# Kernel tuning notes

Hardware: AMD Instinct MI355X
Metric: run time of the kernel (lower is better)

The kernel has to match this reference:

```python
import jax, jax.numpy as jnp
import numpy as np

S, D, H, HD, FF = 4096, 1024, 16, 64, 4096  # seq, d_embed, heads, head_dim, hidden
EPS = 1e-6  # flax LayerNorm default epsilon


def layer_norm(x, scale, bias):
    mu = jnp.mean(x, axis=-1, keepdims=True)
    var = jnp.var(x, axis=-1, keepdims=True)
    return (x - mu) * jax.lax.rsqrt(var + EPS) * scale + bias


def rope(x):
    # x: [S, H, HD]; standard half-split rotary embedding, base 10000
    half = x.shape[-1] // 2
    freq = 1.0 / (10000.0 ** (jnp.arange(half, dtype=x.dtype) / half))  # [half]
    ang = jnp.arange(x.shape[0], dtype=x.dtype)[:, None] * freq          # [S, half]
    cos = jnp.cos(ang)[:, None, :]
    sin = jnp.sin(ang)[:, None, :]
    x1, x2 = x[..., :half], x[..., half:]
    return jnp.concatenate([x1 * cos - x2 * sin, x2 * cos + x1 * sin], axis=-1)


def setup_inputs() -> dict:
    key = jax.random.key(0)
    ks = jax.random.split(key, 8)
    s = 0.02
    return {
        "x": jax.random.normal(ks[0], (S, D), jnp.float32),
        "ln1_scale": jnp.ones((D,), jnp.float32), "ln1_bias": jnp.zeros((D,), jnp.float32),
        "ln2_scale": jnp.ones((D,), jnp.float32), "ln2_bias": jnp.zeros((D,), jnp.float32),
        "Wq": jax.random.normal(ks[1], (D, H, HD), jnp.float32) * s, "bq": jnp.zeros((H, HD), jnp.float32),
        "Wk": jax.random.normal(ks[2], (D, H, HD), jnp.float32) * s, "bk": jnp.zeros((H, HD), jnp.float32),
        "Wv": jax.random.normal(ks[3], (D, H, HD), jnp.float32) * s, "bv": jnp.zeros((H, HD), jnp.float32),
        "Wo": jax.random.normal(ks[4], (H, HD, D), jnp.float32) * s, "bo": jnp.zeros((D,), jnp.float32),
        "W1": jax.random.normal(ks[5], (D, FF), jnp.float32) * s, "b1": jnp.zeros((FF,), jnp.float32),
        "W2": jax.random.normal(ks[6], (FF, D), jnp.float32) * s, "b2": jnp.zeros((D,), jnp.float32),
    }


def reference(x, ln1_scale, ln1_bias, ln2_scale, ln2_bias, Wq, bq, Wk, bk, Wv, bv, Wo, bo, W1, b1, W2, b2):
    # Pre-LN attention block with RoPE fused into QK scores
    y = layer_norm(x, ln1_scale, ln1_bias)
    q = jnp.einsum('sd,dhc->shc', y, Wq) + bq  # [S,H,HD]
    k = jnp.einsum('sd,dhc->shc', y, Wk) + bk
    v = jnp.einsum('sd,dhc->shc', y, Wv) + bv
    q = rope(q)
    k = rope(k)
    scores = jnp.einsum('qhc,khc->hqk', q, k) / jnp.sqrt(jnp.asarray(HD, x.dtype))  # [H,S,S]
    p = jax.nn.softmax(scores, axis=-1)
    o = jnp.einsum('hqk,khc->qhc', p, v)                # [S,H,HD]
    attn_out = jnp.einsum('qhc,hcd->qd', o, Wo) + bo    # [S,D]
    x = x + attn_out
    # Pre-LN GELU MLP block
    y = layer_norm(x, ln2_scale, ln2_bias)
    y = jax.nn.gelu(y @ W1 + b1, approximate=False)
    x = x + (y @ W2 + b2)
    return x
```

## Files before the change

kernel.cpp:

```cpp
#include <hip/hip_runtime.h>
#include <hip/hip_bf16.h>
#include <math.h>

using bf16 = __hip_bfloat16;
typedef __attribute__((ext_vector_type(8))) short short8;
typedef __attribute__((ext_vector_type(4))) short s16x4;
typedef __attribute__((ext_vector_type(4))) float f32x4;

constexpr int S = 4096, D = 1024, H = 16, HD = 64, FF = 4096;

static __device__ __forceinline__ float tof(bf16 v) { return __bfloat162float(v); }
static __device__ __forceinline__ bf16 tob(float v) { return __float2bfloat16(v); }
static __device__ __forceinline__ short tobs(float v) {
    bf16 h = __float2bfloat16(v);
    return *reinterpret_cast<short*>(&h);
}
static __device__ __forceinline__ unsigned pkbf16(float a, float b) {
    __hip_bfloat162 h = __float22bfloat162_rn(make_float2(a, b));
    return *reinterpret_cast<unsigned*>(&h);
}

static __device__ __forceinline__ f32x4 mfma16(short8 a, short8 b, f32x4 c) {
    return __builtin_amdgcn_mfma_f32_16x16x32_bf16(a, b, c, 0, 0, 0);
}
static __device__ __forceinline__ void stage16(const bf16* g, bf16* l) {
    __builtin_amdgcn_global_load_lds((__attribute__((address_space(1))) void*)g,
                                     (__attribute__((address_space(3))) void*)l, 16, 0, 0);
}

__global__ __launch_bounds__(256) void ln_kernel(const float* __restrict__ x,
                                                 const float* __restrict__ scale,
                                                 const float* __restrict__ bias,
                                                 bf16* __restrict__ y) {
    int row = blockIdx.x, t = threadIdx.x;
    const float* xr = x + (size_t)row * D;
    float v[4], s = 0.f, ss = 0.f;
#pragma unroll
    for (int i = 0; i < 4; ++i) {
        v[i] = xr[t + 256 * i];
        s += v[i]; ss += v[i] * v[i];
    }
    __shared__ float r0[256], r1[256];
    r0[t] = s; r1[t] = ss;
    __syncthreads();
    for (int off = 128; off; off >>= 1) {
        if (t < off) { r0[t] += r0[t + off]; r1[t] += r1[t + off]; }
        __syncthreads();
    }
    float mu  = r0[0] * (1.f / D);
    float var = r1[0] * (1.f / D) - mu * mu;
    float inv = rsqrtf(var + 1e-6f);
    bf16* yr = y + (size_t)row * D;
#pragma unroll
    for (int i = 0; i < 4; ++i) {
        int c = t + 256 * i;
        yr[c] = tob((v[i] - mu) * inv * scale[c] + bias[c]);
    }
}

__global__ __launch_bounds__(256) void wtrans(const float* __restrict__ W,
                                              bf16* __restrict__ BT, int K, int N) {
    __shared__ float t[32][33];
    int kt = blockIdx.y * 32, nt = blockIdx.x * 32;
    int tid = threadIdx.x, r = tid >> 5, c = tid & 31;
#pragma unroll
    for (int p = 0; p < 4; ++p)
        t[r + p * 8][c] = W[(size_t)(kt + r + p * 8) * N + nt + c];
    __syncthreads();
#pragma unroll
    for (int p = 0; p < 4; ++p)
        BT[(size_t)(nt + r + p * 8) * K + kt + c] = tob(t[c][r + p * 8]);
}

__global__ __launch_bounds__(256) void wtrans_qkv(const float* __restrict__ Wq,
                                                  const float* __restrict__ Wk,
                                                  const float* __restrict__ Wv,
                                                  bf16* __restrict__ BT) {
    __shared__ float t[32][33];
    const float* W = blockIdx.z == 0 ? Wq : (blockIdx.z == 1 ? Wk : Wv);
    bf16* dst = BT + (size_t)blockIdx.z * 1024 * 1024;
    int kt = blockIdx.y * 32, nt = blockIdx.x * 32;
    int tid = threadIdx.x, r = tid >> 5, c = tid & 31;
#pragma unroll
    for (int p = 0; p < 4; ++p)
        t[r + p * 8][c] = W[(size_t)(kt + r + p * 8) * 1024 + nt + c];
    __syncthreads();
#pragma unroll
    for (int p = 0; p < 4; ++p)
        dst[(size_t)(nt + r + p * 8) * 1024 + kt + c] = tob(t[c][r + p * 8]);
}

__global__ void bconcat(const float* __restrict__ bq, const float* __restrict__ bk,
                        const float* __restrict__ bv, float* __restrict__ out) {
    int i = blockIdx.x * 256 + threadIdx.x;
    out[i] = i < 1024 ? bq[i] : (i < 2048 ? bk[i - 1024] : bv[i - 2048]);
}

#define EPI_NONE 0
#define EPI_RES  1
#define EPI_GELU 2

template <int EPI, int MT>
__global__ __launch_bounds__(256, MT == 128 ? 2 : 3) void gemm_bt(
    const bf16* __restrict__ A, const bf16* __restrict__ BT,
    const float* __restrict__ bias, const float* resid, void* out,
    int M, int N, int K) {
    constexpr int NJ = (MT == 128) ? 4 : 2;
    __shared__ bf16 As[MT * 32];
    __shared__ bf16 Bs[128 * 32];
    const int tid = threadIdx.x;
    const int w = tid >> 6, lane = tid & 63;
    const int quad = lane >> 4, l16 = lane & 15;
    const int rowBase = blockIdx.y * MT, colBase = blockIdx.x * 128;
    const int wr = (MT == 128) ? (w >> 1) * 64 : 0;
    const int wc = (MT == 128) ? (w & 1) * 64 : w * 32;
    const int sr = lane >> 2, skb = (lane & 3) * 8;
    f32x4 acc[4][NJ] = {};
    for (int k0 = 0; k0 < K; k0 += 32) {
        __syncthreads();
        if (MT == 128) {
#pragma unroll
            for (int t = 0; t < 2; ++t) {
                int inst = w * 2 + t;
                int r = inst * 16 + sr;
                stage16(A  + (size_t)(rowBase + r) * K + k0 + skb, As + inst * 512);
                stage16(BT + (size_t)(colBase + r) * K + k0 + skb, Bs + inst * 512);
            }
        } else {
            stage16(A + (size_t)(rowBase + w * 16 + sr) * K + k0 + skb, As + w * 512);
#pragma unroll
            for (int t = 0; t < 2; ++t) {
                int inst = w + t * 4;
                stage16(BT + (size_t)(colBase + inst * 16 + sr) * K + k0 + skb, Bs + inst * 512);
            }
        }
        __syncthreads();
        const bf16* pa = As + (wr + l16) * 32 + quad * 8;
        const bf16* pb = Bs + (wc + l16) * 32 + quad * 8;
        short8 a[4], b[NJ];
#pragma unroll
        for (int i = 0; i < 4; ++i) a[i] = *(const short8*)(pa + i * 512);
#pragma unroll
        for (int j = 0; j < NJ; ++j) b[j] = *(const short8*)(pb + j * 512);
#pragma unroll
        for (int i = 0; i < 4; ++i)
#pragma unroll
            for (int j = 0; j < NJ; ++j) acc[i][j] = mfma16(a[i], b[j], acc[i][j]);
    }
#pragma unroll
    for (int j = 0; j < NJ; ++j) {
        int c = colBase + wc + j * 16 + l16;
        float bj = bias[c];
#pragma unroll
        for (int i = 0; i < 4; ++i) {
            int r0 = rowBase + wr + i * 16 + quad * 4;
#pragma unroll
            for (int reg = 0; reg < 4; ++reg) {
                size_t idx = (size_t)(r0 + reg) * N + c;
                float val = acc[i][j][reg] + bj;
                if (EPI == EPI_NONE) {
                    ((bf16*)out)[idx] = tob(val);
                } else if (EPI == EPI_RES) {
                    ((float*)out)[idx] = val + resid[idx];
                } else {
                    float g = 0.5f * val * (1.f + erff(val * 0.70710678118f));
                    ((bf16*)out)[idx] = tob(g);
                }
            }
        }
    }
}

__global__ __launch_bounds__(256) void rope_kernel(bf16* __restrict__ QKV) {
    int idx = blockIdx.x * 256 + threadIdx.x;
    int s = idx >> 9, rem = idx & 511, h = rem >> 5, c = rem & 31;
    float freq = __expf(-(float)c * (9.210340371976184f / 32.f));
    float ang = (float)s * freq, sn, cs;
    sincosf(ang, &sn, &cs);
    const float qs = 0.125f * 1.44269504088896f;
    size_t base = (size_t)s * 3072 + h * 64 + c;
    float q1 = tof(QKV[base]), q2 = tof(QKV[base + 32]);
    QKV[base]      = tob((q1 * cs - q2 * sn) * qs);
    QKV[base + 32] = tob((q2 * cs + q1 * sn) * qs);
    float k1 = tof(QKV[base + 1024]), k2 = tof(QKV[base + 1056]);
    QKV[base + 1024] = tob(k1 * cs - k2 * sn);
    QKV[base + 1056] = tob(k2 * cs + k1 * sn);
}

__global__ __launch_bounds__(256) void vtrans(const short* __restrict__ QKV,
                                              short* __restrict__ VT) {
    int h = blockIdx.y, st = blockIdx.x * 64;
    __shared__ short t[64][72];
    int tid = threadIdx.x, r0 = tid >> 3, c0 = (tid & 7) * 8;
#pragma unroll
    for (int p = 0; p < 2; ++p) {
        int r = r0 + p * 32;
        short8 d = *(const short8*)(QKV + (size_t)(st + r) * 3072 + 2048 + h * 64 + c0);
#pragma unroll
        for (int j = 0; j < 8; ++j) t[r][c0 + j] = d[j];
    }
    __syncthreads();
#pragma unroll
    for (int p = 0; p < 2; ++p) {
        int c = r0 + p * 32;
        short8 v;
#pragma unroll
        for (int j = 0; j < 8; ++j) v[j] = t[c0 + j][c];
        *(short8*)(VT + ((size_t)h * 64 + c) * 4096 + st + c0) = v;
    }
}

__global__ __launch_bounds__(256, 4) void attn_kernel(const bf16* __restrict__ QKV,
                                                      const bf16* __restrict__ VT,
                                                      bf16* __restrict__ O) {
    const int h = blockIdx.x >> 6, qb = blockIdx.x & 63;
    const int w = threadIdx.x >> 6, lane = threadIdx.x & 63;
    const int quad = lane >> 4, l16 = lane & 15;
    const int q0w = qb * 64 + w * 16;
    const bf16* Qh = QKV + h * 64;
    const bf16* Kh = QKV + 1024 + h * 64;
    const bf16* Vh = VT + (size_t)h * 64 * 4096;

    __shared__ char smem[24576];
    bf16* Ks = (bf16*)(smem);
    bf16* Vs = (bf16*)(smem + 8192);
    char* Pb = smem + 16384 + w * 2048;

    const int sw = l16 & 7;
    const int rloc = lane >> 3, slot = lane & 7;
    const int schunk = (slot ^ rloc) * 8;

    short8 qf[2];
#pragma unroll
    for (int c = 0; c < 2; ++c)
        qf[c] = *(const short8*)(Qh + (size_t)(q0w + l16) * 3072 + c * 32 + quad * 8);

    const short ob = (l16 == 0) ? (short)0x3F80 : (short)0;
    const short8 ones8 = {ob, ob, ob, ob, ob, ob, ob, ob};

    f32x4 acc[4] = {};
    f32x4 accl = {};
    const f32x4 zero = {0.f, 0.f, 0.f, 0.f};

    for (int kt = 0; kt < 4096; kt += 64) {
        __syncthreads();
        {
            int r = (2 * w ) * 8 + rloc;
            stage16(Kh + (size_t)(kt + r) * 3072 + schunk, Ks + 2 * w * 512);
            stage16(Vh + (size_t)r * 4096 + kt + schunk, Vs + 2 * w * 512);
            int r1 = (2 * w + 1) * 8 + rloc;
            stage16(Kh + (size_t)(kt + r1) * 3072 + schunk, Ks + (2 * w + 1) * 512);
            stage16(Vh + (size_t)r1 * 4096 + kt + schunk, Vs + (2 * w + 1) * 512);
        }
        __syncthreads();

        f32x4 st[4];
#pragma unroll
        for (int nt = 0; nt < 4; ++nt) {
            const bf16* kr = Ks + (nt * 16 + l16) * 64;
            short8 k0 = *(const short8*)(kr + ((quad ^ sw) * 8));
            short8 k1 = *(const short8*)(kr + (((quad + 4) ^ sw) * 8));
            st[nt] = mfma16(k1, qf[1], mfma16(k0, qf[0], zero));
        }
#pragma unroll
        for (int nt = 0; nt < 4; ++nt) {
            float e0 = exp2f(st[nt][0]), e1 = exp2f(st[nt][1]);
            float e2 = exp2f(st[nt][2]), e3 = exp2f(st[nt][3]);
            uint2 pk = {pkbf16(e0, e1), pkbf16(e2, e3)};
            *(uint2*)(Pb + l16 * 128 + (((nt * 2 + (quad >> 1)) ^ sw) * 16) + (quad & 1) * 8) = pk;
        }
        asm volatile("s_waitcnt lgkmcnt(0)" ::: "memory");
#pragma unroll
        for (int c = 0; c < 2; ++c) {
            short8 pB = *(const short8*)(Pb + l16 * 128 + (((c * 4 + quad) ^ sw) * 16));
            accl = mfma16(ones8, pB, accl);
#pragma unroll
            for (int vt = 0; vt < 4; ++vt) {
                short8 vf = *(const short8*)(Vs + (vt * 16 + l16) * 64 + (((c * 4 + quad) ^ sw) * 8));
                acc[vt] = mfma16(vf, pB, acc[vt]);
            }
        }
    }
    float linv = 1.f / __shfl(accl[0], l16, 64);
#pragma unroll
    for (int vt = 0; vt < 4; ++vt) {
        s16x4 ov = {tobs(acc[vt][0] * linv), tobs(acc[vt][1] * linv),
                    tobs(acc[vt][2] * linv), tobs(acc[vt][3] * linv)};
        *(s16x4*)(O + (size_t)(q0w + l16) * 1024 + h * 64 + vt * 16 + quad * 4) = ov;
    }
}

extern "C" void kernel_launch(void* const* d_in, const int* in_sizes, int n_in,
                              void* d_out, int out_size, void* d_ws, size_t ws_size,
                              hipStream_t stream) {
    const float* x   = (const float*)d_in[0];
    const float* s1  = (const float*)d_in[1];
    const float* b1n = (const float*)d_in[2];
    const float* s2  = (const float*)d_in[3];
    const float* b2n = (const float*)d_in[4];
    const float* Wq  = (const float*)d_in[5];
    const float* bq  = (const float*)d_in[6];
    const float* Wk  = (const float*)d_in[7];
    const float* bk  = (const float*)d_in[8];
    const float* Wv  = (const float*)d_in[9];
    const float* bv  = (const float*)d_in[10];
    const float* Wo  = (const float*)d_in[11];
    const float* bo  = (const float*)d_in[12];
    const float* W1  = (const float*)d_in[13];
    const float* b1  = (const float*)d_in[14];
    const float* W2  = (const float*)d_in[15];
    const float* b2  = (const float*)d_in[16];

    char* ws = (char*)d_ws;
    bf16*  y     = (bf16*)(ws);
    bf16*  QKV   = (bf16*)(ws + (8ull  << 20));
    bf16*  o     = (bf16*)(ws + (32ull << 20));
    bf16*  hb    = (bf16*)(ws + (40ull << 20));
    bf16*  BTqkv = (bf16*)(ws + (40ull << 20));
    bf16*  BTo   = (bf16*)(ws + (46ull << 20));
    bf16*  VT    = (bf16*)(ws + (72ull << 20));
    bf16*  BT1   = (bf16*)(ws + (82ull << 20));
    float* bqkv  = (float*)(ws + (90ull << 20));
    bf16*  BT2   = y;
    float* x1    = (float*)d_out;

    wtrans_qkv<<<dim3(32, 32, 3), 256, 0, stream>>>(Wq, Wk, Wv, BTqkv);
    wtrans<<<dim3(32, 32),  256, 0, stream>>>(Wo, BTo, D, D);
    wtrans<<<dim3(128, 32), 256, 0, stream>>>(W1, BT1, D, FF);
    bconcat<<<12, 256, 0, stream>>>(bq, bk, bv, bqkv);

    ln_kernel<<<S, 256, 0, stream>>>(x, s1, b1n, y);

    gemm_bt<EPI_NONE, 128><<<dim3(24, 32), 256, 0, stream>>>(y, BTqkv, bqkv, nullptr, QKV, S, 3072, D);

    rope_kernel<<<(S * H * 32) / 256, 256, 0, stream>>>(QKV);
    vtrans<<<dim3(64, 16), 256, 0, stream>>>((const short*)QKV, (short*)VT);

    attn_kernel<<<H * 64, 256, 0, stream>>>(QKV, VT, o);

    gemm_bt<EPI_RES, 64><<<dim3(8, 64), 256, 0, stream>>>(o, BTo, bo, x, x1, S, D, D);

    ln_kernel<<<S, 256, 0, stream>>>(x1, s2, b2n, y);

    gemm_bt<EPI_GELU, 128><<<dim3(32, 32), 256, 0, stream>>>(y, BT1, b1, nullptr, hb, S, FF, D);

    wtrans<<<dim3(32, 128), 256, 0, stream>>>(W2, BT2, FF, D);
    gemm_bt<EPI_RES, 64><<<dim3(8, 64), 256, 0, stream>>>(hb, BT2, b2, x1, d_out, S, D, FF);
}
```

Baseline: 477.8 us.

## Fuse RoPE and V transpose into QKV GEMM, double-buffer attention, merge weight transposes

Applies rotary embedding and the V transpose directly in the QKV GEMM epilogue, removing two separate kernels and their extra passes over the QKV buffer. All weight transposes and the bias concat become a single launch. The attention loop double-buffers K/V tiles in shared memory so loads overlap compute, at the cost of more LDS, and uses the hardware exp2 intrinsic. The epilogue now does per-element sincos and strided stores, which may add epilogue cost.

```diff
diff --git a/kernel.cpp b/kernel.cpp
--- a/kernel.cpp
+++ b/kernel.cpp
@@ -19,6 +19,12 @@
     __hip_bfloat162 h = __float22bfloat162_rn(make_float2(a, b));
     return *reinterpret_cast<unsigned*>(&h);
 }
+
+#if __has_builtin(__builtin_amdgcn_exp2f)
+#define EXP2(x) __builtin_amdgcn_exp2f(x)
+#else
+#define EXP2(x) exp2f(x)
+#endif
 
 static __device__ __forceinline__ f32x4 mfma16(short8 a, short8 b, f32x4 c) {
     return __builtin_amdgcn_mfma_f32_16x16x32_bf16(a, b, c, 0, 0, 0);
@@ -58,10 +64,29 @@
     }
 }
 
-__global__ __launch_bounds__(256) void wtrans(const float* __restrict__ W,
-                                              bf16* __restrict__ BT, int K, int N) {
+__global__ __launch_bounds__(256) void wtrans_all(
+    const float* __restrict__ Wq, const float* __restrict__ Wk,
+    const float* __restrict__ Wv, const float* __restrict__ Wo,
+    const float* __restrict__ W1, const float* __restrict__ W2,
+    const float* __restrict__ bq, const float* __restrict__ bk,
+    const float* __restrict__ bv,
+    bf16* __restrict__ BTqkv, bf16* __restrict__ BTo,
+    bf16* __restrict__ BT1, bf16* __restrict__ BT2, float* __restrict__ bqkv) {
+    int id = blockIdx.x;
+    if (id >= 12288) {
+        int i = (id - 12288) * 256 + threadIdx.x;
+        bqkv[i] = i < 1024 ? bq[i] : (i < 2048 ? bk[i - 1024] : bv[i - 2048]);
+        return;
+    }
+    const float* W; bf16* dst; int K, N, local;
+    if (id < 3072)      { int s = id >> 10; W = s == 0 ? Wq : (s == 1 ? Wk : Wv);
+                          dst = BTqkv + (size_t)s * 1048576; K = 1024; N = 1024; local = id & 1023; }
+    else if (id < 4096) { W = Wo; dst = BTo; K = 1024; N = 1024; local = id - 3072; }
+    else if (id < 8192) { W = W1; dst = BT1; K = 1024; N = 4096; local = id - 4096; }
+    else                { W = W2; dst = BT2; K = 4096; N = 1024; local = id - 8192; }
+    int ls = (N == 4096) ? 7 : 5;
+    int nt = (local & ((1 << ls) - 1)) << 5, kt = (local >> ls) << 5;
     __shared__ float t[32][33];
-    int kt = blockIdx.y * 32, nt = blockIdx.x * 32;
     int tid = threadIdx.x, r = tid >> 5, c = tid & 31;
 #pragma unroll
     for (int p = 0; p < 4; ++p)
@@ -69,41 +94,17 @@
     __syncthreads();
 #pragma unroll
     for (int p = 0; p < 4; ++p)
-        BT[(size_t)(nt + r + p * 8) * K + kt + c] = tob(t[c][r + p * 8]);
-}
-
-__global__ __launch_bounds__(256) void wtrans_qkv(const float* __restrict__ Wq,
-                                                  const float* __restrict__ Wk,
-                                                  const float* __restrict__ Wv,
-                                                  bf16* __restrict__ BT) {
-    __shared__ float t[32][33];
-    const float* W = blockIdx.z == 0 ? Wq : (blockIdx.z == 1 ? Wk : Wv);
-    bf16* dst = BT + (size_t)blockIdx.z * 1024 * 1024;
-    int kt = blockIdx.y * 32, nt = blockIdx.x * 32;
-    int tid = threadIdx.x, r = tid >> 5, c = tid & 31;
-#pragma unroll
-    for (int p = 0; p < 4; ++p)
-        t[r + p * 8][c] = W[(size_t)(kt + r + p * 8) * 1024 + nt + c];
-    __syncthreads();
-#pragma unroll
-    for (int p = 0; p < 4; ++p)
-        dst[(size_t)(nt + r + p * 8) * 1024 + kt + c] = tob(t[c][r + p * 8]);
-}
-
-__global__ void bconcat(const float* __restrict__ bq, const float* __restrict__ bk,
-                        const float* __restrict__ bv, float* __restrict__ out) {
-    int i = blockIdx.x * 256 + threadIdx.x;
-    out[i] = i < 1024 ? bq[i] : (i < 2048 ? bk[i - 1024] : bv[i - 2048]);
-}
-
-#define EPI_NONE 0
+        dst[(size_t)(nt + r + p * 8) * K + kt + c] = tob(t[c][r + p * 8]);
+}
+
 #define EPI_RES  1
 #define EPI_GELU 2
+#define EPI_QKV  3
 
 template <int EPI, int MT>
 __global__ __launch_bounds__(256, MT == 128 ? 2 : 3) void gemm_bt(
     const bf16* __restrict__ A, const bf16* __restrict__ BT,
-    const float* __restrict__ bias, const float* resid, void* out,
+    const float* __restrict__ bias, const float* resid, void* out, void* out2,
     int M, int N, int K) {
     constexpr int NJ = (MT == 128) ? 4 : 2;
     __shared__ bf16 As[MT * 32];
@@ -147,66 +148,68 @@
 #pragma unroll
             for (int j = 0; j < NJ; ++j) acc[i][j] = mfma16(a[i], b[j], acc[i][j]);
     }
-#pragma unroll
-    for (int j = 0; j < NJ; ++j) {
-        int c = colBase + wc + j * 16 + l16;
-        float bj = bias[c];
-#pragma unroll
-        for (int i = 0; i < 4; ++i) {
-            int r0 = rowBase + wr + i * 16 + quad * 4;
-#pragma unroll
-            for (int reg = 0; reg < 4; ++reg) {
-                size_t idx = (size_t)(r0 + reg) * N + c;
-                float val = acc[i][j][reg] + bj;
-                if (EPI == EPI_NONE) {
-                    ((bf16*)out)[idx] = tob(val);
-                } else if (EPI == EPI_RES) {
-                    ((float*)out)[idx] = val + resid[idx];
-                } else {
-                    float g = 0.5f * val * (1.f + erff(val * 0.70710678118f));
-                    ((bf16*)out)[idx] = tob(g);
+    if (EPI == EPI_QKV) {
+        bf16* QKVo = (bf16*)out;
+        bf16* VTo  = (bf16*)out2;
+        if (colBase >= 2048) {
+#pragma unroll
+            for (int j = 0; j < NJ; ++j) {
+                int c = colBase + wc + j * 16 + l16;
+                float bj = bias[c];
+                size_t cc = (size_t)(c - 2048) * 4096;
+#pragma unroll
+                for (int i = 0; i < 4; ++i) {
+                    int r0 = rowBase + wr + i * 16 + quad * 4;
+                    s16x4 ov = {tobs(acc[i][j][0] + bj), tobs(acc[i][j][1] + bj),
+                                tobs(acc[i][j][2] + bj), tobs(acc[i][j][3] + bj)};
+                    *(s16x4*)(VTo + cc + r0) = ov;
                 }
             }
-        }
-    }
-}
-
-__global__ __launch_bounds__(256) void rope_kernel(bf16* __restrict__ QKV) {
-    int idx = blockIdx.x * 256 + threadIdx.x;
-    int s = idx >> 9, rem = idx & 511, h = rem >> 5, c = rem & 31;
-    float freq = __expf(-(float)c * (9.210340371976184f / 32.f));
-    float ang = (float)s * freq, sn, cs;
-    sincosf(ang, &sn, &cs);
-    const float qs = 0.125f * 1.44269504088896f;
-    size_t base = (size_t)s * 3072 + h * 64 + c;
-    float q1 = tof(QKV[base]), q2 = tof(QKV[base + 32]);
-    QKV[base]      = tob((q1 * cs - q2 * sn) * qs);
-    QKV[base + 32] = tob((q2 * cs + q1 * sn) * qs);
-    float k1 = tof(QKV[base + 1024]), k2 = tof(QKV[base + 1056]);
-    QKV[base + 1024] = tob(k1 * cs - k2 * sn);
-    QKV[base + 1056] = tob(k2 * cs + k1 * sn);
-}
-
-__global__ __launch_bounds__(256) void vtrans(const short* __restrict__ QKV,
-                                              short* __restrict__ VT) {
-    int h = blockIdx.y, st = blockIdx.x * 64;
-    __shared__ short t[64][72];
-    int tid = threadIdx.x, r0 = tid >> 3, c0 = (tid & 7) * 8;
-#pragma unroll
-    for (int p = 0; p < 2; ++p) {
-        int r = r0 + p * 32;
-        short8 d = *(const short8*)(QKV + (size_t)(st + r) * 3072 + 2048 + h * 64 + c0);
-#pragma unroll
-        for (int j = 0; j < 8; ++j) t[r][c0 + j] = d[j];
-    }
-    __syncthreads();
-#pragma unroll
-    for (int p = 0; p < 2; ++p) {
-        int c = r0 + p * 32;
-        short8 v;
-#pragma unroll
-        for (int j = 0; j < 8; ++j) v[j] = t[c0 + j][c];
-        *(short8*)(VT + ((size_t)h * 64 + c) * 4096 + st + c0) = v;
+        } else {
+            const bool isq = colBase < 1024;
+            const float qs = isq ? 0.125f * 1.44269504088896f : 1.f;
+#pragma unroll
+            for (int j2 = 0; j2 < 2; ++j2) {
+                int dim = j2 * 16 + l16;
+                float freq = __expf(-(float)dim * (9.210340371976184f / 32.f));
+                int c1 = colBase + wc + j2 * 16 + l16, c2 = c1 + 32;
+                float b1v = bias[c1], b2v = bias[c2];
+#pragma unroll
+                for (int i = 0; i < 4; ++i) {
+#pragma unroll
+                    for (int reg = 0; reg < 4; ++reg) {
+                        int s = rowBase + wr + i * 16 + quad * 4 + reg;
+                        float sn, cs;
+                        sincosf((float)s * freq, &sn, &cs);
+                        float x1 = acc[i][j2][reg] + b1v;
+                        float x2 = acc[i][j2 + 2][reg] + b2v;
+                        QKVo[(size_t)s * 3072 + c1] = tob((x1 * cs - x2 * sn) * qs);
+                        QKVo[(size_t)s * 3072 + c2] = tob((x2 * cs + x1 * sn) * qs);
+                    }
+                }
+            }
+        }
+    } else {
+#pragma unroll
+        for (int j = 0; j < NJ; ++j) {
+            int c = colBase + wc + j * 16 + l16;
+            float bj = bias[c];
+#pragma unroll
+            for (int i = 0; i < 4; ++i) {
+                int r0 = rowBase + wr + i * 16 + quad * 4;
+#pragma unroll
+                for (int reg = 0; reg < 4; ++reg) {
+                    size_t idx = (size_t)(r0 + reg) * N + c;
+                    float val = acc[i][j][reg] + bj;
+                    if (EPI == EPI_RES) {
+                        ((float*)out)[idx] = val + resid[idx];
+                    } else {
+                        float g = 0.5f * val * (1.f + erff(val * 0.70710678118f));
+                        ((bf16*)out)[idx] = tob(g);
+                    }
+                }
+            }
+        }
     }
 }
 
@@ -221,14 +224,19 @@
     const bf16* Kh = QKV + 1024 + h * 64;
     const bf16* Vh = VT + (size_t)h * 64 * 4096;
 
-    __shared__ char smem[24576];
+    __shared__ char smem[40960];
     bf16* Ks = (bf16*)(smem);
-    bf16* Vs = (bf16*)(smem + 8192);
-    char* Pb = smem + 16384 + w * 2048;
+    bf16* Vs = (bf16*)(smem + 16384);
+    char* Pb = smem + 32768 + w * 2048;
 
     const int sw = l16 & 7;
     const int rloc = lane >> 3, slot = lane & 7;
     const int schunk = (slot ^ rloc) * 8;
+    const int row0 = 2 * w * 8 + rloc, row1 = (2 * w + 1) * 8 + rloc;
+    const size_t kOff0 = (size_t)row0 * 3072 + schunk;
+    const size_t kOff1 = (size_t)row1 * 3072 + schunk;
+    const size_t vOff0 = (size_t)row0 * 4096 + schunk;
+    const size_t vOff1 = (size_t)row1 * 4096 + schunk;
 
     short8 qf[2];
 #pragma unroll
@@ -242,30 +250,30 @@
     f32x4 accl = {};
     const f32x4 zero = {0.f, 0.f, 0.f, 0.f};
 
-    for (int kt = 0; kt < 4096; kt += 64) {
-        __syncthreads();
-        {
-            int r = (2 * w ) * 8 + rloc;
-            stage16(Kh + (size_t)(kt + r) * 3072 + schunk, Ks + 2 * w * 512);
-            stage16(Vh + (size_t)r * 4096 + kt + schunk, Vs + 2 * w * 512);
-            int r1 = (2 * w + 1) * 8 + rloc;
-            stage16(Kh + (size_t)(kt + r1) * 3072 + schunk, Ks + (2 * w + 1) * 512);
-            stage16(Vh + (size_t)r1 * 4096 + kt + schunk, Vs + (2 * w + 1) * 512);
-        }
-        __syncthreads();
-
+    auto stage = [&](int sel, int kt) {
+        bf16* kd = Ks + sel * 4096 + 2 * w * 512;
+        bf16* vd = Vs + sel * 4096 + 2 * w * 512;
+        const bf16* kb = Kh + (size_t)kt * 3072;
+        stage16(kb + kOff0, kd);
+        stage16(kb + kOff1, kd + 512);
+        stage16(Vh + vOff0 + kt, vd);
+        stage16(Vh + vOff1 + kt, vd + 512);
+    };
+    auto compute = [&](int sel) {
+        const bf16* Kt = Ks + sel * 4096;
+        const bf16* Vt = Vs + sel * 4096;
         f32x4 st[4];
 #pragma unroll
         for (int nt = 0; nt < 4; ++nt) {
-            const bf16* kr = Ks + (nt * 16 + l16) * 64;
+            const bf16* kr = Kt + (nt * 16 + l16) * 64;
             short8 k0 = *(const short8*)(kr + ((quad ^ sw) * 8));
             short8 k1 = *(const short8*)(kr + (((quad + 4) ^ sw) * 8));
             st[nt] = mfma16(k1, qf[1], mfma16(k0, qf[0], zero));
         }
 #pragma unroll
         for (int nt = 0; nt < 4; ++nt) {
-            float e0 = exp2f(st[nt][0]), e1 = exp2f(st[nt][1]);
-            float e2 = exp2f(st[nt][2]), e3 = exp2f(st[nt][3]);
+            float e0 = EXP2(st[nt][0]), e1 = EXP2(st[nt][1]);
+            float e2 = EXP2(st[nt][2]), e3 = EXP2(st[nt][3]);
             uint2 pk = {pkbf16(e0, e1), pkbf16(e2, e3)};
             *(uint2*)(Pb + l16 * 128 + (((nt * 2 + (quad >> 1)) ^ sw) * 16) + (quad & 1) * 8) = pk;
         }
@@ -276,11 +284,22 @@
             accl = mfma16(ones8, pB, accl);
 #pragma unroll
             for (int vt = 0; vt < 4; ++vt) {
-                short8 vf = *(const short8*)(Vs + (vt * 16 + l16) * 64 + (((c * 4 + quad) ^ sw) * 8));
+                short8 vf = *(const short8*)(Vt + (vt * 16 + l16) * 64 + (((c * 4 + quad) ^ sw) * 8));
                 acc[vt] = mfma16(vf, pB, acc[vt]);
             }
         }
-    }
+    };
+
+    stage(0, 0);
+    for (int kt = 0; kt < 4096; kt += 128) {
+        __syncthreads();
+        stage(1, kt + 64);
+        compute(0);
+        __syncthreads();
+        if (kt + 128 < 4096) stage(0, kt + 128);
+        compute(1);
+    }
+
     float linv = 1.f / __shfl(accl[0], l16, 64);
 #pragma unroll
     for (int vt = 0; vt < 4; ++vt) {
@@ -319,31 +338,25 @@
     bf16*  BTqkv = (bf16*)(ws + (40ull << 20));
     bf16*  BTo   = (bf16*)(ws + (46ull << 20));
     bf16*  VT    = (bf16*)(ws + (72ull << 20));
-    bf16*  BT1   = (bf16*)(ws + (82ull << 20));
-    float* bqkv  = (float*)(ws + (90ull << 20));
-    bf16*  BT2   = y;
+    bf16*  BT1   = (bf16*)(ws + (80ull << 20));
+    bf16*  BT2   = (bf16*)(ws + (88ull << 20));
+    float* bqkv  = (float*)(ws + (32ull << 20));
     float* x1    = (float*)d_out;
 
-    wtrans_qkv<<<dim3(32, 32, 3), 256, 0, stream>>>(Wq, Wk, Wv, BTqkv);
-    wtrans<<<dim3(32, 32),  256, 0, stream>>>(Wo, BTo, D, D);
-    wtrans<<<dim3(128, 32), 256, 0, stream>>>(W1, BT1, D, FF);
-    bconcat<<<12, 256, 0, stream>>>(bq, bk, bv, bqkv);
+    wtrans_all<<<12300, 256, 0, stream>>>(Wq, Wk, Wv, Wo, W1, W2, bq, bk, bv,
+                                          BTqkv, BTo, BT1, BT2, bqkv);
 
     ln_kernel<<<S, 256, 0, stream>>>(x, s1, b1n, y);
 
-    gemm_bt<EPI_NONE, 128><<<dim3(24, 32), 256, 0, stream>>>(y, BTqkv, bqkv, nullptr, QKV, S, 3072, D);
-
-    rope_kernel<<<(S * H * 32) / 256, 256, 0, stream>>>(QKV);
-    vtrans<<<dim3(64, 16), 256, 0, stream>>>((const short*)QKV, (short*)VT);
+    gemm_bt<EPI_QKV, 128><<<dim3(24, 32), 256, 0, stream>>>(y, BTqkv, bqkv, nullptr, QKV, VT, S, 3072, D);
 
     attn_kernel<<<H * 64, 256, 0, stream>>>(QKV, VT, o);
 
-    gemm_bt<EPI_RES, 64><<<dim3(8, 64), 256, 0, stream>>>(o, BTo, bo, x, x1, S, D, D);
+    gemm_bt<EPI_RES, 64><<<dim3(8, 64), 256, 0, stream>>>(o, BTo, bo, x, x1, nullptr, S, D, D);
 
     ln_kernel<<<S, 256, 0, stream>>>(x1, s2, b2n, y);
 
-    gemm_bt<EPI_GELU, 128><<<dim3(32, 32), 256, 0, stream>>>(y, BT1, b1, nullptr, hb, S, FF, D);
-
-    wtrans<<<dim3(32, 128), 256, 0, stream>>>(W2, BT2, FF, D);
-    gemm_bt<EPI_RES, 64><<<dim3(8, 64), 256, 0, stream>>>(hb, BT2, b2, x1, d_out, S, D, FF);
-}
+    gemm_bt<EPI_GELU, 128><<<dim3(32, 32), 256, 0, stream>>>(y, BT1, b1, nullptr, hb, nullptr, S, FF, D);
+
+    gemm_bt<EPI_RES, 64><<<dim3(8, 64), 256, 0, stream>>>(hb, BT2, b2, x1, d_out, nullptr, S, D, FF);
+}
```

Result: faster. 433.2 us (-9.3%).
